# Kernel tuning notes

Hardware: AMD Instinct MI355X
Metric: run time of the kernel (lower is better)

## Reference

```python
import jax, jax.numpy as jnp
import numpy as np

L, H, N, F, E, FF, OUT, B = 4, 8, 1024, 128, 128, 512, 64, 32


def setup_inputs() -> dict:
    key = jax.random.key(0)
    ks = jax.random.split(key, 16)
    s = 0.02
    return {
        "x": jax.random.normal(ks[0], (B, N, F), jnp.float32),
        "adj": jax.random.randint(ks[1], (N, N), 0, 2, jnp.int32),
        "Ws": jax.random.normal(ks[2], (L, H, E, F), jnp.float32) * s,
        "bs": jnp.zeros((L, H, E), jnp.float32),
        "As": jax.random.normal(ks[3], (L, H, 2 * E, N), jnp.float32) * s,
        "W1": jax.random.normal(ks[4], (L, FF, F), jnp.float32) * s,
        "b1": jnp.zeros((L, FF), jnp.float32),
        "W2": jax.random.normal(ks[5], (L, F, FF), jnp.float32) * s,
        "b2": jnp.zeros((L, F), jnp.float32),
        "g1": jnp.ones((L, F), jnp.float32),
        "be1": jnp.zeros((L, F), jnp.float32),
        "g2": jnp.ones((L, F), jnp.float32),
        "be2": jnp.zeros((L, F), jnp.float32),
        "Wo": jax.random.normal(ks[6], (OUT, N * F), jnp.float32) * s,
        "bo": jnp.zeros((OUT,), jnp.float32),
    }


def _ln(x, g, b, eps=1e-5):
    m = jnp.mean(x, axis=-1, keepdims=True)
    v = jnp.mean((x - m) ** 2, axis=-1, keepdims=True)
    return (x - m) / jnp.sqrt(v + eps) * g + b


def reference(x, adj, Ws, bs, As, W1, b1, W2, b2, g1, be1, g2, be2, Wo, bo):
    # mask[j, i] = 1 if j is a neighbor of i (adj_matrix[:, i] > 0 in torch source)
    mask = (adj > 0).astype(x.dtype)
    E_ = Ws.shape[2]
    for l in range(Ws.shape[0]):
        # per-head projection: h [B, H, N, E]
        h = jnp.einsum('bnf,hef->bhne', x, Ws[l]) + bs[l][None, :, None, :]
        # score[b,h,i] = h_i . a[:E, i] + (sum_{j in N(i)} h_j) . a[E:, i]
        s1 = jnp.einsum('bhne,hen->bhn', h, As[l][:, :E_, :])
        hn = jnp.einsum('jn,bhje->bhne', mask, h)  # neighbor sums
        s2 = jnp.einsum('bhne,hen->bhn', hn, As[l][:, E_:, :])
        score = s1 + s2  # [B, H, N]
        # attention row i is the constant score[b,h,i] broadcast over columns,
        # so attention @ h == score[...,None] * h.sum(over nodes)
        hsum = h.sum(axis=2)  # [B, H, E]
        hp = score[..., None] * hsum[:, :, None, :]  # [B, H, N, E]
        att = jax.nn.leaky_relu(hp, 0.01).sum(axis=1)  # sum over heads -> [B, N, F]
        x = _ln(x + att, g1[l], be1[l])
        ff = jax.nn.relu(x @ W1[l].T + b1[l]) @ W2[l].T + b2[l]
        x = _ln(x + ff, g2[l], be2[l])
    flat = x.reshape(x.shape[0], -1)  # [B, N*F]
    return jax.nn.relu(flat) @ Wo.T + bo
```

## Files before the change

### kernel.cpp

```cpp
#include <hip/hip_runtime.h>

#define L_ 4
#define H_ 8
#define Nn 1024
#define F_ 128
#define E_ 128
#define FF_ 512
#define OUT_ 64
#define B_ 32
#define KTOT (Nn * F_)

typedef unsigned short u16;
typedef __bf16 bf16_t;
typedef __attribute__((ext_vector_type(8))) __bf16 bf16x8;
typedef __attribute__((ext_vector_type(4))) float f32x4;

__device__ __forceinline__ u16 f2b(float v) {
    bf16_t h = (bf16_t)v;
    return __builtin_bit_cast(u16, h);
}

typedef const __attribute__((address_space(1))) void* gvp;
typedef __attribute__((address_space(3))) void* lvp;
__device__ __forceinline__ void gll16(const void* g, void* l) {
    __builtin_amdgcn_global_load_lds((gvp)g, (lvp)l, 16, 0, 0);
}

template <int R>
__device__ __forceinline__ void stage(const u16* __restrict__ g, int ldg,
                                      u16* lds, int w, int l) {
    const int r8 = l >> 3, jq = l & 7;
#pragma unroll
    for (int i = 0; i < R / 32; ++i) {
        const int row0 = w * (R / 4) + i * 8;
        const int row = row0 + r8;
        gll16(g + (long)row * ldg + ((jq ^ (row & 7)) << 3), lds + row0 * 64);
    }
}

template <int BM, int BN, bool DUAL, int EPI, int BSH, bool GSWAP, bool DBUF>
__global__ __launch_bounds__(256) void k_mfma(
    const u16* __restrict__ A, int lda, long sAz,
    const u16* __restrict__ Bhp, const u16* __restrict__ Blp, int ldb, long sBz,
    const float* __restrict__ bias,
    float* __restrict__ Cf, u16* __restrict__ Cb, int ldc, long sCz, int K)
{
    constexpr int WN = (BN == 64) ? 1 : ((BM == 64) ? 4 : 2);
    constexpr int WM = 4 / WN;
    constexpr int SM = BM / WM, SN = BN / WN;
    constexpr int MF = SM / 16, NF = SN / 16;
    constexpr int BUFE = BM * 64 + (DUAL ? 2 : 1) * BN * 64;
    __shared__ __align__(16) u16 lds[BUFE * (DBUF ? 2 : 1)];
    const int t = threadIdx.x;
    const int w = t >> 6, l = t & 63, lr = l & 15, lg = l >> 4;
    const int wm0 = (w / WN) * SM, wn0 = (w % WN) * SN;
    const int bidm = GSWAP ? blockIdx.z : blockIdx.x;
    const int bidz = GSWAP ? blockIdx.x : blockIdx.z;
    const int m0 = bidm * BM, n0 = blockIdx.y * BN;
    A += BSH ? ((long)(bidz >> 1) * sAz + (long)(bidz & 1) * 128)
             : (long)bidz * sAz;
    Bhp += (long)(bidz >> BSH) * sBz;
    if (DUAL) Blp += (long)bidz * sBz;

    f32x4 acc[MF][NF] = {};

    auto stageAll = [&](u16* base, int k0) {
        stage<BM>(A + (long)m0 * lda + k0, lda, base, w, l);
        stage<BN>(Bhp + (long)n0 * ldb + k0, ldb, base + BM * 64, w, l);
        if (DUAL) stage<BN>(Blp + (long)n0 * ldb + k0, ldb, base + BM * 64 + BN * 64, w, l);
    };
    auto compute = [&](const u16* base) {
        const u16* Al = base;
        const u16* Bh = base + BM * 64;
        const u16* Bl = Bh + BN * 64;
#pragma unroll
        for (int ks = 0; ks < 2; ++ks) {
            bf16x8 af[MF], bh[NF], bl[NF];
            const int kq = ks * 4 + lg;
#pragma unroll
            for (int mf = 0; mf < MF; ++mf) {
                int row = wm0 + mf * 16 + lr;
                af[mf] = *reinterpret_cast<const bf16x8*>(&Al[row * 64 + ((kq ^ (row & 7)) << 3)]);
            }
#pragma unroll
            for (int nf = 0; nf < NF; ++nf) {
                int row = wn0 + nf * 16 + lr;
                int off = row * 64 + ((kq ^ (row & 7)) << 3);
                bh[nf] = *reinterpret_cast<const bf16x8*>(&Bh[off]);
                if (DUAL) bl[nf] = *reinterpret_cast<const bf16x8*>(&Bl[off]);
            }
#pragma unroll
            for (int mf = 0; mf < MF; ++mf)
#pragma unroll
                for (int nf = 0; nf < NF; ++nf) {
                    acc[mf][nf] = __builtin_amdgcn_mfma_f32_16x16x32_bf16(af[mf], bh[nf], acc[mf][nf], 0, 0, 0);
                    if (DUAL)
                        acc[mf][nf] = __builtin_amdgcn_mfma_f32_16x16x32_bf16(af[mf], bl[nf], acc[mf][nf], 0, 0, 0);
                }
        }
    };

    if (DBUF) {
        stageAll(lds, 0);
        __syncthreads();
        int cur = 0;
        for (int k0 = 0; k0 < K; k0 += 64) {
            if (k0 + 64 < K) stageAll(lds + (cur ^ 1) * BUFE, k0 + 64);
            compute(lds + cur * BUFE);
            __syncthreads();
            cur ^= 1;
        }
    } else {
        for (int k0 = 0; k0 < K; k0 += 64) {
            __syncthreads();
            stageAll(lds, k0);
            __syncthreads();
            compute(lds);
        }
    }

    float bv[NF];
    if (EPI) {
#pragma unroll
        for (int nf = 0; nf < NF; ++nf) bv[nf] = bias[n0 + wn0 + nf * 16 + lr];
    }
    if (EPI == 1) Cb += (long)bidz * sCz;
    else          Cf += (long)bidz * sCz;
#pragma unroll
    for (int mf = 0; mf < MF; ++mf)
#pragma unroll
        for (int nf = 0; nf < NF; ++nf)
#pragma unroll
            for (int r = 0; r < 4; ++r) {
                long row = m0 + wm0 + mf * 16 + lg * 4 + r;
                int col = n0 + wn0 + nf * 16 + lr;
                float v = acc[mf][nf][r];
                if (EPI) v += bv[nf];
                if (EPI == 1) Cb[row * ldc + col] = f2b(fmaxf(v, 0.f));
                else          Cf[row * ldc + col] = v;
            }
}

template <bool LAST>
__global__ __launch_bounds__(256) void k_ff_ln2(
    const u16* __restrict__ xb,
    const u16* __restrict__ W1b,
    const float* __restrict__ b1,
    const u16* __restrict__ W2b,
    const float* __restrict__ b2,
    float* __restrict__ xc,
    const float* __restrict__ g, const float* __restrict__ be,
    u16* __restrict__ xh, u16* __restrict__ xl,
    float* __restrict__ xsp,
    u16* __restrict__ xrb)
{
    __shared__ __align__(16) u16 lds[32768];
    const int t = threadIdx.x;
    const int w = t >> 6, l = t & 63, lr = l & 15, lg = l >> 4;
    const int wn0 = w * 32;
    const int m0 = blockIdx.x * 64;
    u16* A0 = lds;
    u16* P0 = lds + 8192;
    u16* W0 = lds + 16384;

    stage<64>(xb + (long)m0 * F_,      F_, A0, w, l);
    stage<64>(xb + (long)m0 * F_ + 64, F_, A0 + 4096, w, l);

    f32x4 acc2[4][2] = {};
    for (int c = 0; c < 4; ++c) {
        __syncthreads();
        stage<128>(W1b + (long)(c * 128) * F_,      F_, W0, w, l);
        stage<128>(W1b + (long)(c * 128) * F_ + 64, F_, W0 + 8192, w, l);
        __syncthreads();
        f32x4 acc1[4][2] = {};
#pragma unroll
        for (int kh = 0; kh < 2; ++kh) {
            const u16* Ah = A0 + kh * 4096;
            const u16* Wh = W0 + kh * 8192;
#pragma unroll
            for (int ks = 0; ks < 2; ++ks) {
                const int kq = ks * 4 + lg;
                bf16x8 af[4], bfr[2];
#pragma unroll
                for (int mf = 0; mf < 4; ++mf) {
                    int row = mf * 16 + lr;
                    af[mf] = *reinterpret_cast<const bf16x8*>(&Ah[row * 64 + ((kq ^ (row & 7)) << 3)]);
                }
#pragma unroll
                for (int nf = 0; nf < 2; ++nf) {
                    int row = wn0 + nf * 16 + lr;
                    bfr[nf] = *reinterpret_cast<const bf16x8*>(&Wh[row * 64 + ((kq ^ (row & 7)) << 3)]);
                }
#pragma unroll
                for (int mf = 0; mf < 4; ++mf)
#pragma unroll
                    for (int nf = 0; nf < 2; ++nf)
                        acc1[mf][nf] = __builtin_amdgcn_mfma_f32_16x16x32_bf16(af[mf], bfr[nf], acc1[mf][nf], 0, 0, 0);
            }
        }
        float b1v[2] = { b1[c * 128 + wn0 + lr], b1[c * 128 + wn0 + 16 + lr] };
#pragma unroll
        for (int mf = 0; mf < 4; ++mf)
#pragma unroll
            for (int nf = 0; nf < 2; ++nf)
#pragma unroll
                for (int r = 0; r < 4; ++r) {
                    int row = mf * 16 + lg * 4 + r;
                    int cc = wn0 + nf * 16 + lr;
                    int c6 = cc & 63;
                    float v = fmaxf(acc1[mf][nf][r] + b1v[nf], 0.f);
                    P0[(cc >> 6) * 4096 + row * 64 + ((((c6 >> 3) ^ (row & 7))) << 3) + (c6 & 7)] = f2b(v);
                }
        __syncthreads();
        stage<128>(W2b + c * 128,      FF_, W0, w, l);
        stage<128>(W2b + c * 128 + 64, FF_, W0 + 8192, w, l);
        __syncthreads();
#pragma unroll
        for (int kh = 0; kh < 2; ++kh) {
            const u16* Ph = P0 + kh * 4096;
            const u16* Wh = W0 + kh * 8192;
#pragma unroll
            for (int ks = 0; ks < 2; ++ks) {
                const int kq = ks * 4 + lg;
                bf16x8 af[4], bfr[2];
#pragma unroll
                for (int mf = 0; mf < 4; ++mf) {
                    int row = mf * 16 + lr;
                    af[mf] = *reinterpret_cast<const bf16x8*>(&Ph[row * 64 + ((kq ^ (row & 7)) << 3)]);
                }
#pragma unroll
                for (int nf = 0; nf < 2; ++nf) {
                    int row = wn0 + nf * 16 + lr;
                    bfr[nf] = *reinterpret_cast<const bf16x8*>(&Wh[row * 64 + ((kq ^ (row & 7)) << 3)]);
                }
#pragma unroll
                for (int mf = 0; mf < 4; ++mf)
#pragma unroll
                    for (int nf = 0; nf < 2; ++nf)
                        acc2[mf][nf] = __builtin_amdgcn_mfma_f32_16x16x32_bf16(af[mf], bfr[nf], acc2[mf][nf], 0, 0, 0);
            }
        }
    }
    __syncthreads();
    float (*buf)[132] = (float(*)[132])lds;
    float (*ps)[128]  = (float(*)[128])((char*)lds + 34816);
    float bv[2] = { b2[wn0 + lr], b2[wn0 + 16 + lr] };
#pragma unroll
    for (int mf = 0; mf < 4; ++mf)
#pragma unroll
        for (int nf = 0; nf < 2; ++nf)
#pragma unroll
            for (int r = 0; r < 4; ++r)
                buf[mf * 16 + lg * 4 + r][wn0 + nf * 16 + lr] = acc2[mf][nf][r] + bv[nf];
    __syncthreads();
    const float gl0 = g[l], gl1 = g[l + 64], bl0 = be[l], bl1 = be[l + 64];
    float s0 = 0.f, s1 = 0.f;
#pragma unroll
    for (int rr = 0; rr < 16; ++rr) {
        const int row = w * 16 + rr;
        const long xb_ = (long)(m0 + row) * F_;
        float v0 = buf[row][l] + xc[xb_ + l];
        float v1 = buf[row][l + 64] + xc[xb_ + l + 64];
        float sum = v0 + v1;
#pragma unroll
        for (int o = 32; o; o >>= 1) sum += __shfl_xor(sum, o);
        const float mean = sum * (1.f / 128.f);
        const float d0 = v0 - mean, d1 = v1 - mean;
        float vs = d0 * d0 + d1 * d1;
#pragma unroll
        for (int o = 32; o; o >>= 1) vs += __shfl_xor(vs, o);
        const float rstd = rsqrtf(vs * (1.f / 128.f) + 1e-5f);
        float o0 = d0 * rstd * gl0 + bl0;
        float o1 = d1 * rstd * gl1 + bl1;
        if (LAST) {
            xrb[xb_ + l] = f2b(fmaxf(o0, 0.f));
            xrb[xb_ + l + 64] = f2b(fmaxf(o1, 0.f));
        } else {
            xc[xb_ + l] = o0;       xc[xb_ + l + 64] = o1;
            buf[row][l] = o0;       buf[row][l + 64] = o1;
            s0 += o0;               s1 += o1;
        }
    }
    if (!LAST) {
        ps[w][l] = s0; ps[w][l + 64] = s1;
        __syncthreads();
        const int b = m0 >> 10, nb0 = m0 & 1023, seg = (m0 >> 6) & 15;
        const int n8 = (t & 7) * 8, fb = t >> 3;
#pragma unroll
        for (int i = 0; i < 4; ++i) {
            const int f = fb + 32 * i;
            union { u16 u[8]; float4 v; } Hv, Lv;
#pragma unroll
            for (int j = 0; j < 8; ++j) {
                float v = buf[n8 + j][f];
                bf16_t h = (bf16_t)v;
                Hv.u[j] = __builtin_bit_cast(u16, h);
                Lv.u[j] = f2b(v - (float)h);
            }
            const long ob = ((long)b * F_ + f) * Nn + nb0 + n8;
            *reinterpret_cast<float4*>(&xh[ob]) = Hv.v;
            *reinterpret_cast<float4*>(&xl[ob]) = Lv.v;
        }
        if (t < 128)
            xsp[((long)b * 16 + seg) * 128 + t] =
                ps[0][t] + ps[1][t] + ps[2][t] + ps[3][t];
    }
}

__global__ __launch_bounds__(256) void k_final_mfma(
    const u16* __restrict__ xrb, const u16* __restrict__ Wob,
    float* __restrict__ part)
{
    __shared__ __align__(16) u16 Al[32 * 512];
    const int c = blockIdx.x;
    const long k0 = (long)c * 512;
    const int t = threadIdx.x, w = t >> 6, l = t & 63, lr = l & 15, lg = l >> 4;
#pragma unroll
    for (int i = 0; i < 8; ++i) {
        int ch = i * 256 + t, row = ch >> 6, jq = ch & 63;
        *reinterpret_cast<float4*>(&Al[row * 512 + ((jq ^ (row & 7)) << 3)]) =
            *reinterpret_cast<const float4*>(&xrb[(long)row * KTOT + k0 + (jq << 3)]);
    }
    __syncthreads();
    f32x4 acc[2] = {};
    const u16* Bp = Wob + (long)(w * 16 + lr) * KTOT + k0 + lg * 8;
#pragma unroll
    for (int ks = 0; ks < 16; ++ks) {
        bf16x8 bfr = *reinterpret_cast<const bf16x8*>(Bp + ks * 32);
        const int j8 = ks * 4 + lg;
#pragma unroll
        for (int mf = 0; mf < 2; ++mf) {
            int row = mf * 16 + lr;
            bf16x8 af = *reinterpret_cast<const bf16x8*>(&Al[row * 512 + ((j8 ^ (row & 7)) << 3)]);
            acc[mf] = __builtin_amdgcn_mfma_f32_16x16x32_bf16(af, bfr, acc[mf], 0, 0, 0);
        }
    }
#pragma unroll
    for (int mf = 0; mf < 2; ++mf)
#pragma unroll
        for (int r = 0; r < 4; ++r) {
            int b = mf * 16 + lg * 4 + r, o = w * 16 + lr;
            part[((long)c * B_ + b) * OUT_ + o] = acc[mf][r];
        }
}

__global__ void k_final_reduce(const float* __restrict__ part,
                               const float* __restrict__ bo, float* __restrict__ out)
{
    int i = blockIdx.x * 256 + threadIdx.x;
    int o = i & 63;
    float s = bo[o];
    for (int c = 0; c < 256; ++c) s += part[(long)c * (B_ * OUT_) + i];
    out[i] = s;
}

__global__ __launch_bounds__(256) void k_maskT(const int* __restrict__ adj,
                                               u16* __restrict__ maskTb,
                                               int* __restrict__ degi)
{
    __shared__ u16 tl[64][65];
    const int j0 = blockIdx.x * 64, n0 = blockIdx.y * 64, t = threadIdx.x;
#pragma unroll
    for (int i = 0; i < 16; ++i) {
        int s = i * 256 + t, jl = s >> 6, nl = s & 63;
        tl[jl][nl] = (adj[(long)(j0 + jl) * Nn + n0 + nl] > 0) ? 0x3F80 : 0;
    }
    __syncthreads();
    if (t < 64) {
        int c = 0;
#pragma unroll
        for (int jl = 0; jl < 64; ++jl) c += (tl[jl][t] != 0);
        atomicAdd(&degi[n0 + t], c);
    }
#pragma unroll
    for (int i = 0; i < 16; ++i) {
        int s = i * 256 + t, nl = s >> 6, jl = s & 63;
        maskTb[(long)(n0 + nl) * Nn + j0 + jl] = tl[jl][nl];
    }
}

__global__ __launch_bounds__(256) void k_tpb(const float* __restrict__ in,
                                             u16* __restrict__ out, int R, int C)
{
    __shared__ float tl[64][65];
    const int c0 = blockIdx.x * 64, r0 = blockIdx.y * 64, t = threadIdx.x;
    in  += (long)blockIdx.z * R * C;
    out += (long)blockIdx.z * R * C;
#pragma unroll
    for (int i = 0; i < 16; ++i) {
        int s = i * 256 + t, rl = s >> 6, cl = s & 63;
        tl[rl][cl] = in[(long)(r0 + rl) * C + c0 + cl];
    }
    __syncthreads();
#pragma unroll
    for (int i = 0; i < 16; ++i) {
        int s = i * 256 + t, cl = s >> 6, rl = s & 63;
        out[(long)(c0 + cl) * R + r0 + rl] = f2b(tl[rl][cl]);
    }
}

__global__ void k_cvtW(const float* __restrict__ W1, const float* __restrict__ W2,
                       u16* __restrict__ W1b, u16* __restrict__ W2b)
{
    int i = blockIdx.x * 256 + threadIdx.x;
    W1b[i] = f2b(W1[i]);
    W2b[i] = f2b(W2[i]);
}

__global__ void k_cvtWo(const float* __restrict__ Wo, u16* __restrict__ Wob)
{
    long i = ((long)blockIdx.x * 256 + threadIdx.x) * 8;
    float4 a = *reinterpret_cast<const float4*>(&Wo[i]);
    float4 b = *reinterpret_cast<const float4*>(&Wo[i + 4]);
    union { u16 u[8]; float4 v; } r;
    r.u[0] = f2b(a.x); r.u[1] = f2b(a.y); r.u[2] = f2b(a.z); r.u[3] = f2b(a.w);
    r.u[4] = f2b(b.x); r.u[5] = f2b(b.y); r.u[6] = f2b(b.z); r.u[7] = f2b(b.w);
    *reinterpret_cast<float4*>(&Wob[i]) = r.v;
}

__global__ __launch_bounds__(256) void k_xpose(const float* __restrict__ x,
                                               u16* __restrict__ xh, u16* __restrict__ xl)
{
    __shared__ float tile[64][132];
    const int b = blockIdx.y, n0 = blockIdx.x * 64, t = threadIdx.x;
#pragma unroll
    for (int i = 0; i < 8; ++i) {
        int s = i * 256 + t, nl = s >> 5, f4 = (s & 31) << 2;
        float4 v = *reinterpret_cast<const float4*>(&x[((long)b * Nn + n0 + nl) * F_ + f4]);
        tile[nl][f4] = v.x; tile[nl][f4 + 1] = v.y;
        tile[nl][f4 + 2] = v.z; tile[nl][f4 + 3] = v.w;
    }
    __syncthreads();
    const int f = t >> 1, nb = (t & 1) << 5;
    const long ob = ((long)b * F_ + f) * Nn + n0 + nb;
    union { u16 u[8]; float4 v; } Hv, Lv;
#pragma unroll
    for (int i = 0; i < 32; i += 8) {
#pragma unroll
        for (int j = 0; j < 8; ++j) {
            float v = tile[nb + i + j][f];
            bf16_t h = (bf16_t)v;
            Hv.u[j] = __builtin_bit_cast(u16, h);
            Lv.u[j] = f2b(v - (float)h);
        }
        *reinterpret_cast<float4*>(&xh[ob + i]) = Hv.v;
        *reinterpret_cast<float4*>(&xl[ob + i]) = Lv.v;
    }
}

__global__ __launch_bounds__(256) void k_xs2(const float* __restrict__ x, float* __restrict__ xsp)
{
    __shared__ float sh[2][128];
    const int seg = blockIdx.x, b = blockIdx.y, t = threadIdx.x;
    const int f = t & 127, h2 = t >> 7;
    const float* p = x + ((long)b * Nn + seg * 64 + h2 * 32) * F_ + f;
    float s = 0.f;
    for (int i = 0; i < 32; ++i) s += p[(long)i * F_];
    sh[h2][f] = s;
    __syncthreads();
    if (t < 128) xsp[((long)b * 16 + seg) * 128 + t] = sh[0][t] + sh[1][t];
}

__global__ void k_hsum(const float* __restrict__ xsp, const float* __restrict__ Wl,
                       const float* __restrict__ bsl, float* __restrict__ hsum)
{
    __shared__ float xs[128];
    const int i = blockIdx.x * 256 + threadIdx.x;
    const int b = i >> 10;
    if (threadIdx.x < 128) {
        const float* xp = xsp + (long)b * 16 * 128 + threadIdx.x;
        float v = 0.f;
#pragma unroll
        for (int sg = 0; sg < 16; ++sg) v += xp[sg * 128];
        xs[threadIdx.x] = v;
    }
    __syncthreads();
    const int e = i & 127, h = (i >> 7) & 7;
    const float* w = Wl + ((long)h * E_ + e) * F_;
    float s = 0.f;
    for (int f = 0; f < F_; ++f) s += xs[f] * w[f];
    hsum[i] = s + (float)Nn * bsl[h * E_ + e];
}

__global__ void k_d12(const float* __restrict__ As, const float* __restrict__ bs,
                      float* __restrict__ d12all)
{
    const int lyr = blockIdx.y;
    const float* Asl = As + (long)lyr * H_ * 2 * E_ * Nn;
    const float* bsl = bs + (long)lyr * H_ * E_;
    int i = blockIdx.x * 256 + threadIdx.x;
    int n = i & 1023, h = (i >> 10) & 7, w = i >> 13;
    const float* a = Asl + ((long)h * 2 * E_ + (long)w * E_) * Nn + n;
    const float* bb = bsl + h * E_;
    float s = 0.f;
    for (int e = 0; e < E_; ++e) s += bb[e] * a[(long)e * Nn];
    d12all[(long)lyr * 2 * H_ * Nn + ((long)w * H_ + h) * Nn + n] = s;
}

__global__ __launch_bounds__(256) void k_score_ln1(
    float* __restrict__ x, const float* __restrict__ y,
    const float* __restrict__ Ct, const float* __restrict__ d12,
    const int* __restrict__ degi, const float* __restrict__ hsum,
    const float* __restrict__ g, const float* __restrict__ be,
    u16* __restrict__ xb)
{
    const int n = blockIdx.x, t = threadIdx.x;
    __shared__ float c1[H_][128], c2[H_][128];
    __shared__ float sbs[H_];
#pragma unroll
    for (int i = 0; i < 4; ++i) {
        int s = i * 256 + t, h = s >> 7, f = s & 127;
        c1[h][f] = Ct[((long)(2 * h) * Nn + n) * F_ + f];
        c2[h][f] = Ct[((long)(2 * h + 1) * Nn + n) * F_ + f];
    }
    if (t < H_) sbs[t] = d12[(long)t * Nn + n] + (float)degi[n] * d12[(long)(H_ + t) * Nn + n];
    __syncthreads();
    const int w = t >> 6, l = t & 63;
    const float gl0 = g[l], gl1 = g[l + 64], bl0 = be[l], bl1 = be[l + 64];
    for (int bi = 0; bi < 8; ++bi) {
        const int b = w * 8 + bi;
        const long base = ((long)b * Nn + n) * F_;
        float x0 = x[base + l], x1 = x[base + l + 64];
        float y0 = y[base + l], y1 = y[base + l + 64];
        float a0 = 0.f, a1 = 0.f;
#pragma unroll
        for (int h = 0; h < H_; ++h) {
            float p = x0 * c1[h][l] + x1 * c1[h][l + 64]
                    + y0 * c2[h][l] + y1 * c2[h][l + 64];
#pragma unroll
            for (int o = 32; o; o >>= 1) p += __shfl_xor(p, o);
            float s = p + sbs[h];
            float h0 = hsum[((long)b * H_ + h) * E_ + l];
            float h1 = hsum[((long)b * H_ + h) * E_ + l + 64];
            float p0 = s * h0, p1 = s * h1;
            a0 += (p0 > 0.f ? p0 : 0.01f * p0);
            a1 += (p1 > 0.f ? p1 : 0.01f * p1);
        }
        float v0 = x0 + a0, v1 = x1 + a1;
        float sum = v0 + v1;
#pragma unroll
        for (int o = 32; o; o >>= 1) sum += __shfl_xor(sum, o);
        const float mean = sum * (1.f / 128.f);
        const float d0 = v0 - mean, d1 = v1 - mean;
        float vs = d0 * d0 + d1 * d1;
#pragma unroll
        for (int o = 32; o; o >>= 1) vs += __shfl_xor(vs, o);
        const float rstd = rsqrtf(vs * (1.f / 128.f) + 1e-5f);
        float o0 = d0 * rstd * gl0 + bl0;
        float o1 = d1 * rstd * gl1 + bl1;
        x[base + l] = o0;        x[base + l + 64] = o1;
        xb[base + l] = f2b(o0);  xb[base + l + 64] = f2b(o1);
    }
}

extern "C" void kernel_launch(void* const* d_in, const int* in_sizes, int n_in,
                              void* d_out, int out_size, void* d_ws, size_t ws_size,
                              hipStream_t stream)
{
    const float* x_in = (const float*)d_in[0];
    const int*   adj  = (const int*)d_in[1];
    const float* Ws   = (const float*)d_in[2];
    const float* bs   = (const float*)d_in[3];
    const float* As   = (const float*)d_in[4];
    const float* W1   = (const float*)d_in[5];
    const float* b1   = (const float*)d_in[6];
    const float* W2   = (const float*)d_in[7];
    const float* b2   = (const float*)d_in[8];
    const float* g1   = (const float*)d_in[9];
    const float* be1  = (const float*)d_in[10];
    const float* g2   = (const float*)d_in[11];
    const float* be2  = (const float*)d_in[12];
    const float* Wo   = (const float*)d_in[13];
    const float* bo   = (const float*)d_in[14];
    float* out = (float*)d_out;

    char* wsb = (char*)d_ws;
    u16*   maskTb = (u16*)wsb;
    float* xc     = (float*)(wsb + (2L << 20));
    float* y      = (float*)(wsb + (18L << 20));
    float* CtAll  = (float*)(wsb + (66L << 20));
    u16*   xb     = (u16*)(wsb + (98L << 20));
    u16*   xrb    = (u16*)(wsb + (106L << 20));
    u16*   Wob    = (u16*)(wsb + (114L << 20));
    float* part   = (float*)(wsb + (130L << 20));
    u16*   xTh    = (u16*)(wsb + (132L << 20));
    u16*   xTl    = (u16*)(wsb + (140L << 20));
    u16*   AsTb   = (u16*)(wsb + (148L << 20));
    u16*   WsTb   = (u16*)(wsb + (164L << 20));
    char*  S      = wsb + (166L << 20);
    int*   degi   = (int*)S;
    float* xsp    = (float*)(S + (4L << 10));
    float* hsum   = (float*)(S + (260L << 10));
    float* d12all = (float*)(S + (388L << 10));
    u16*   W1b    = (u16*)(S + (644L << 10));
    u16*   W2b    = (u16*)(S + (1156L << 10));

    hipMemsetAsync(degi, 0, Nn * sizeof(int), stream);
    hipMemcpyAsync(xc, x_in, sizeof(float) * (long)B_ * Nn * F_,
                   hipMemcpyDeviceToDevice, stream);
    k_maskT<<<dim3(16, 16), 256, 0, stream>>>(adj, maskTb, degi);
    k_cvtW<<<(L_ * FF_ * F_) / 256, 256, 0, stream>>>(W1, W2, W1b, W2b);
    k_cvtWo<<<(OUT_ * KTOT) / (256 * 8), 256, 0, stream>>>(Wo, Wob);
    k_tpb<<<dim3(16, 4, L_ * H_), 256, 0, stream>>>(As, AsTb, 2 * E_, Nn);
    k_tpb<<<dim3(2, 2, L_ * H_), 256, 0, stream>>>(Ws, WsTb, E_, F_);
    k_xpose<<<dim3(16, B_), 256, 0, stream>>>(x_in, xTh, xTl);
    k_xs2<<<dim3(16, B_), 256, 0, stream>>>(x_in, xsp);
    k_d12<<<dim3((2 * H_ * Nn) / 256, L_), 256, 0, stream>>>(As, bs, d12all);
    k_mfma<64, 128, false, 0, 1, false, false><<<dim3(16, 1, 64), 256, 0, stream>>>(
        AsTb, 2 * E_, (long)Nn * 2 * E_, WsTb, nullptr, E_, (long)F_ * E_,
        nullptr, CtAll, nullptr, F_, (long)Nn * F_, E_);

    for (int l = 0; l < L_; ++l) {
        const float* Wl  = Ws + (long)l * H_ * E_ * F_;
        const float* bsl = bs + (long)l * H_ * E_;

        k_mfma<128, 64, true, 0, 0, true, true><<<dim3(32, 2, 8), 256, 0, stream>>>(
            maskTb, Nn, 0L, xTh, xTl, Nn, (long)F_ * Nn,
            nullptr, y, nullptr, F_, (long)Nn * F_, Nn);

        k_hsum<<<(B_ * H_ * E_) / 256, 256, 0, stream>>>(xsp, Wl, bsl, hsum);
        k_score_ln1<<<Nn, 256, 0, stream>>>(
            xc, y, CtAll + (long)l * 16 * Nn * F_, d12all + (long)l * 2 * H_ * Nn,
            degi, hsum, g1 + l * F_, be1 + l * F_, xb);
        if (l < L_ - 1)
            k_ff_ln2<false><<<512, 256, 0, stream>>>(
                xb, W1b + (long)l * FF_ * F_, b1 + l * FF_,
                W2b + (long)l * F_ * FF_, b2 + l * F_, xc,
                g2 + l * F_, be2 + l * F_, xTh, xTl, xsp, nullptr);
        else
            k_ff_ln2<true><<<512, 256, 0, stream>>>(
                xb, W1b + (long)l * FF_ * F_, b1 + l * FF_,
                W2b + (long)l * F_ * FF_, b2 + l * F_, xc,
                g2 + l * F_, be2 + l * F_, nullptr, nullptr, nullptr, xrb);
    }

    k_final_mfma<<<256, 256, 0, stream>>>(xrb, Wob, part);
    k_final_reduce<<<(B_ * OUT_) / 256, 256, 0, stream>>>(part, bo, out);
}
```

Measured before the change: 394.2 us.

## Prefetch FFN weight tiles into registers to overlap with MFMA compute

Replaces the synchronous LDS staging of W1/W2 tiles in the fused FFN kernel with a register prefetch. The next weight tile is loaded from global memory into registers while the current GEMM runs, then written to LDS after a barrier, so global load latency hides behind the matrix-multiply work. It also changes the XOR swizzle on the P buffer to mix in row>>3, which should reduce LDS bank conflicts. The cost is higher register pressure from 8 float4 prefetch registers, which may lower occupancy, plus some reordering of barriers.

```diff
diff --git a/kernel.cpp b/kernel.cpp
--- a/kernel.cpp
+++ b/kernel.cpp
@@ -162,16 +162,39 @@
     u16* A0 = lds;
     u16* P0 = lds + 8192;
     u16* W0 = lds + 16384;
+    const int r8 = l >> 3, jq = l & 7;
+
+    float4 wreg[8];
+    auto loadW = [&](const u16* Wsrc, int ld) {
+#pragma unroll
+        for (int h = 0; h < 2; ++h)
+#pragma unroll
+            for (int i = 0; i < 4; ++i) {
+                int row = w * 32 + i * 8 + r8;
+                wreg[h * 4 + i] = *reinterpret_cast<const float4*>(
+                    &Wsrc[(long)row * ld + h * 64 + ((jq ^ (row & 7)) << 3)]);
+            }
+    };
+    auto writeW = [&]() {
+#pragma unroll
+        for (int h = 0; h < 2; ++h)
+#pragma unroll
+            for (int i = 0; i < 4; ++i) {
+                int row0 = w * 32 + i * 8;
+                *reinterpret_cast<float4*>(&W0[h * 8192 + row0 * 64 + l * 8]) = wreg[h * 4 + i];
+            }
+    };
 
     stage<64>(xb + (long)m0 * F_,      F_, A0, w, l);
     stage<64>(xb + (long)m0 * F_ + 64, F_, A0 + 4096, w, l);
+    loadW(W1b, F_);
+    __syncthreads();
+    writeW();
 
     f32x4 acc2[4][2] = {};
     for (int c = 0; c < 4; ++c) {
         __syncthreads();
-        stage<128>(W1b + (long)(c * 128) * F_,      F_, W0, w, l);
-        stage<128>(W1b + (long)(c * 128) * F_ + 64, F_, W0 + 8192, w, l);
-        __syncthreads();
+        loadW(W2b + c * 128, FF_);
         f32x4 acc1[4][2] = {};
 #pragma unroll
         for (int kh = 0; kh < 2; ++kh) {
@@ -198,6 +221,8 @@
                         acc1[mf][nf] = __builtin_amdgcn_mfma_f32_16x16x32_bf16(af[mf], bfr[nf], acc1[mf][nf], 0, 0, 0);
             }
         }
+        __syncthreads();
+        writeW();
         float b1v[2] = { b1[c * 128 + wn0 + lr], b1[c * 128 + wn0 + 16 + lr] };
 #pragma unroll
         for (int mf = 0; mf < 4; ++mf)
@@ -206,14 +231,13 @@
 #pragma unroll
                 for (int r = 0; r < 4; ++r) {
                     int row = mf * 16 + lg * 4 + r;
+                    int sp = (row ^ (row >> 3)) & 7;
                     int cc = wn0 + nf * 16 + lr;
                     int c6 = cc & 63;
                     float v = fmaxf(acc1[mf][nf][r] + b1v[nf], 0.f);
-                    P0[(cc >> 6) * 4096 + row * 64 + ((((c6 >> 3) ^ (row & 7))) << 3) + (c6 & 7)] = f2b(v);
+                    P0[(cc >> 6) * 4096 + row * 64 + (((c6 >> 3) ^ sp) << 3) + (c6 & 7)] = f2b(v);
                 }
-        __syncthreads();
-        stage<128>(W2b + c * 128,      FF_, W0, w, l);
-        stage<128>(W2b + c * 128 + 64, FF_, W0 + 8192, w, l);
+        if (c < 3) loadW(W1b + (long)(c + 1) * 128 * F_, F_);
         __syncthreads();
 #pragma unroll
         for (int kh = 0; kh < 2; ++kh) {
@@ -226,7 +250,8 @@
 #pragma unroll
                 for (int mf = 0; mf < 4; ++mf) {
                     int row = mf * 16 + lr;
-                    af[mf] = *reinterpret_cast<const bf16x8*>(&Ph[row * 64 + ((kq ^ (row & 7)) << 3)]);
+                    int sp = (row ^ (row >> 3)) & 7;
+                    af[mf] = *reinterpret_cast<const bf16x8*>(&Ph[row * 64 + ((kq ^ sp) << 3)]);
                 }
 #pragma unroll
                 for (int nf = 0; nf < 2; ++nf) {
@@ -240,8 +265,9 @@
                         acc2[mf][nf] = __builtin_amdgcn_mfma_f32_16x16x32_bf16(af[mf], bfr[nf], acc2[mf][nf], 0, 0, 0);
             }
         }
-    }
-    __syncthreads();
+        __syncthreads();
+        if (c < 3) writeW();
+    }
     float (*buf)[132] = (float(*)[132])lds;
     float (*ps)[128]  = (float(*)[128])((char*)lds + 34816);
     float bv[2] = { b2[wn0 + lr], b2[wn0 + 16 + lr] };
```

Result: slower. 497.7 us (+26.3%).

## Drop split-bf16 low part for neighbor-sum GEMM and store its output in bf16

Applied to the files above, without the earlier changes.

The mask-times-x neighbor-sum GEMM previously used a hi/lo bf16 split of x, doubling the MFMA work and the transposed-x traffic. It now uses only the bf16 high part, drops the xTl buffer from the transpose and LN2 kernels, and writes the result y as bf16 instead of fp32, which halves its store and load traffic. The LDS swizzle for the P tile in the FF kernel is also changed to reduce bank conflicts. The cost is lower accuracy in the neighbor sums, which may push the output closer to the tolerance limit.

```diff
diff --git a/kernel.cpp b/kernel.cpp
--- a/kernel.cpp
+++ b/kernel.cpp
@@ -18,6 +18,10 @@
 __device__ __forceinline__ u16 f2b(float v) {
     bf16_t h = (bf16_t)v;
     return __builtin_bit_cast(u16, h);
+}
+__device__ __forceinline__ float b2f(u16 u) {
+    unsigned v = (unsigned)u << 16;
+    return __builtin_bit_cast(float, v);
 }
 
 typedef const __attribute__((address_space(1))) void* gvp;
@@ -120,12 +124,12 @@
     }
 
     float bv[NF];
-    if (EPI) {
+    if (EPI == 1) {
 #pragma unroll
         for (int nf = 0; nf < NF; ++nf) bv[nf] = bias[n0 + wn0 + nf * 16 + lr];
     }
-    if (EPI == 1) Cb += (long)bidz * sCz;
-    else          Cf += (long)bidz * sCz;
+    if (EPI == 1 || EPI == 3) Cb += (long)bidz * sCz;
+    else                      Cf += (long)bidz * sCz;
 #pragma unroll
     for (int mf = 0; mf < MF; ++mf)
 #pragma unroll
@@ -135,9 +139,9 @@
                 long row = m0 + wm0 + mf * 16 + lg * 4 + r;
                 int col = n0 + wn0 + nf * 16 + lr;
                 float v = acc[mf][nf][r];
-                if (EPI) v += bv[nf];
-                if (EPI == 1) Cb[row * ldc + col] = f2b(fmaxf(v, 0.f));
-                else          Cf[row * ldc + col] = v;
+                if (EPI == 1) Cb[row * ldc + col] = f2b(fmaxf(v + bv[nf], 0.f));
+                else if (EPI == 3) Cb[row * ldc + col] = f2b(v);
+                else Cf[row * ldc + col] = v;
             }
 }
 
@@ -150,7 +154,7 @@
     const float* __restrict__ b2,
     float* __restrict__ xc,
     const float* __restrict__ g, const float* __restrict__ be,
-    u16* __restrict__ xh, u16* __restrict__ xl,
+    u16* __restrict__ xh,
     float* __restrict__ xsp,
     u16* __restrict__ xrb)
 {
@@ -206,10 +210,11 @@
 #pragma unroll
                 for (int r = 0; r < 4; ++r) {
                     int row = mf * 16 + lg * 4 + r;
+                    int sp = (row ^ (row >> 3)) & 7;
                     int cc = wn0 + nf * 16 + lr;
                     int c6 = cc & 63;
                     float v = fmaxf(acc1[mf][nf][r] + b1v[nf], 0.f);
-                    P0[(cc >> 6) * 4096 + row * 64 + ((((c6 >> 3) ^ (row & 7))) << 3) + (c6 & 7)] = f2b(v);
+                    P0[(cc >> 6) * 4096 + row * 64 + (((c6 >> 3) ^ sp) << 3) + (c6 & 7)] = f2b(v);
                 }
         __syncthreads();
         stage<128>(W2b + c * 128,      FF_, W0, w, l);
@@ -226,7 +231,8 @@
 #pragma unroll
                 for (int mf = 0; mf < 4; ++mf) {
                     int row = mf * 16 + lr;
-                    af[mf] = *reinterpret_cast<const bf16x8*>(&Ph[row * 64 + ((kq ^ (row & 7)) << 3)]);
+                    int sp = (row ^ (row >> 3)) & 7;
+                    af[mf] = *reinterpret_cast<const bf16x8*>(&Ph[row * 64 + ((kq ^ sp) << 3)]);
                 }
 #pragma unroll
                 for (int nf = 0; nf < 2; ++nf) {
@@ -289,17 +295,10 @@
 #pragma unroll
         for (int i = 0; i < 4; ++i) {
             const int f = fb + 32 * i;
-            union { u16 u[8]; float4 v; } Hv, Lv;
-#pragma unroll
-            for (int j = 0; j < 8; ++j) {
-                float v = buf[n8 + j][f];
-                bf16_t h = (bf16_t)v;
-                Hv.u[j] = __builtin_bit_cast(u16, h);
-                Lv.u[j] = f2b(v - (float)h);
-            }
-            const long ob = ((long)b * F_ + f) * Nn + nb0 + n8;
-            *reinterpret_cast<float4*>(&xh[ob]) = Hv.v;
-            *reinterpret_cast<float4*>(&xl[ob]) = Lv.v;
+            union { u16 u[8]; float4 v; } Hv;
+#pragma unroll
+            for (int j = 0; j < 8; ++j) Hv.u[j] = f2b(buf[n8 + j][f]);
+            *reinterpret_cast<float4*>(&xh[((long)b * F_ + f) * Nn + nb0 + n8]) = Hv.v;
         }
         if (t < 128)
             xsp[((long)b * 16 + seg) * 128 + t] =
@@ -419,7 +418,7 @@
 }
 
 __global__ __launch_bounds__(256) void k_xpose(const float* __restrict__ x,
-                                               u16* __restrict__ xh, u16* __restrict__ xl)
+                                               u16* __restrict__ xh)
 {
     __shared__ float tile[64][132];
     const int b = blockIdx.y, n0 = blockIdx.x * 64, t = threadIdx.x;
@@ -433,18 +432,12 @@
     __syncthreads();
     const int f = t >> 1, nb = (t & 1) << 5;
     const long ob = ((long)b * F_ + f) * Nn + n0 + nb;
-    union { u16 u[8]; float4 v; } Hv, Lv;
+    union { u16 u[8]; float4 v; } Hv;
 #pragma unroll
     for (int i = 0; i < 32; i += 8) {
 #pragma unroll
-        for (int j = 0; j < 8; ++j) {
-            float v = tile[nb + i + j][f];
-            bf16_t h = (bf16_t)v;
-            Hv.u[j] = __builtin_bit_cast(u16, h);
-            Lv.u[j] = f2b(v - (float)h);
-        }
+        for (int j = 0; j < 8; ++j) Hv.u[j] = f2b(tile[nb + i + j][f]);
         *reinterpret_cast<float4*>(&xh[ob + i]) = Hv.v;
-        *reinterpret_cast<float4*>(&xl[ob + i]) = Lv.v;
     }
 }
 
@@ -498,7 +491,7 @@
 }
 
 __global__ __launch_bounds__(256) void k_score_ln1(
-    float* __restrict__ x, const float* __restrict__ y,
+    float* __restrict__ x, const u16* __restrict__ y,
     const float* __restrict__ Ct, const float* __restrict__ d12,
     const int* __restrict__ degi, const float* __restrict__ hsum,
     const float* __restrict__ g, const float* __restrict__ be,
@@ -521,7 +514,7 @@
         const int b = w * 8 + bi;
         const long base = ((long)b * Nn + n) * F_;
         float x0 = x[base + l], x1 = x[base + l + 64];
-        float y0 = y[base + l], y1 = y[base + l + 64];
+        float y0 = b2f(y[base + l]), y1 = b2f(y[base + l + 64]);
         float a0 = 0.f, a1 = 0.f;
 #pragma unroll
         for (int h = 0; h < H_; ++h) {
@@ -577,14 +570,13 @@
     char* wsb = (char*)d_ws;
     u16*   maskTb = (u16*)wsb;
     float* xc     = (float*)(wsb + (2L << 20));
-    float* y      = (float*)(wsb + (18L << 20));
+    u16*   yb     = (u16*)(wsb + (18L << 20));
     float* CtAll  = (float*)(wsb + (66L << 20));
     u16*   xb     = (u16*)(wsb + (98L << 20));
     u16*   xrb    = (u16*)(wsb + (106L << 20));
     u16*   Wob    = (u16*)(wsb + (114L << 20));
     float* part   = (float*)(wsb + (130L << 20));
     u16*   xTh    = (u16*)(wsb + (132L << 20));
-    u16*   xTl    = (u16*)(wsb + (140L << 20));
     u16*   AsTb   = (u16*)(wsb + (148L << 20));
     u16*   WsTb   = (u16*)(wsb + (164L << 20));
     char*  S      = wsb + (166L << 20);
@@ -603,7 +595,7 @@
     k_cvtWo<<<(OUT_ * KTOT) / (256 * 8), 256, 0, stream>>>(Wo, Wob);
     k_tpb<<<dim3(16, 4, L_ * H_), 256, 0, stream>>>(As, AsTb, 2 * E_, Nn);
     k_tpb<<<dim3(2, 2, L_ * H_), 256, 0, stream>>>(Ws, WsTb, E_, F_);
-    k_xpose<<<dim3(16, B_), 256, 0, stream>>>(x_in, xTh, xTl);
+    k_xpose<<<dim3(16, B_), 256, 0, stream>>>(x_in, xTh);
     k_xs2<<<dim3(16, B_), 256, 0, stream>>>(x_in, xsp);
     k_d12<<<dim3((2 * H_ * Nn) / 256, L_), 256, 0, stream>>>(As, bs, d12all);
     k_mfma<64, 128, false, 0, 1, false, false><<<dim3(16, 1, 64), 256, 0, stream>>>(
@@ -614,24 +606,24 @@
         const float* Wl  = Ws + (long)l * H_ * E_ * F_;
         const float* bsl = bs + (long)l * H_ * E_;
 
-        k_mfma<128, 64, true, 0, 0, true, true><<<dim3(32, 2, 8), 256, 0, stream>>>(
-            maskTb, Nn, 0L, xTh, xTl, Nn, (long)F_ * Nn,
-            nullptr, y, nullptr, F_, (long)Nn * F_, Nn);
+        k_mfma<128, 64, false, 3, 0, true, true><<<dim3(32, 2, 8), 256, 0, stream>>>(
+            maskTb, Nn, 0L, xTh, nullptr, Nn, (long)F_ * Nn,
+            nullptr, nullptr, yb, F_, (long)Nn * F_, Nn);
 
         k_hsum<<<(B_ * H_ * E_) / 256, 256, 0, stream>>>(xsp, Wl, bsl, hsum);
         k_score_ln1<<<Nn, 256, 0, stream>>>(
-            xc, y, CtAll + (long)l * 16 * Nn * F_, d12all + (long)l * 2 * H_ * Nn,
+            xc, yb, CtAll + (long)l * 16 * Nn * F_, d12all + (long)l * 2 * H_ * Nn,
             degi, hsum, g1 + l * F_, be1 + l * F_, xb);
         if (l < L_ - 1)
             k_ff_ln2<false><<<512, 256, 0, stream>>>(
                 xb, W1b + (long)l * FF_ * F_, b1 + l * FF_,
                 W2b + (long)l * F_ * FF_, b2 + l * F_, xc,
-                g2 + l * F_, be2 + l * F_, xTh, xTl, xsp, nullptr);
+                g2 + l * F_, be2 + l * F_, xTh, xsp, nullptr);
         else
             k_ff_ln2<true><<<512, 256, 0, stream>>>(
                 xb, W1b + (long)l * FF_ * F_, b1 + l * FF_,
                 W2b + (long)l * F_ * FF_, b2 + l * F_, xc,
-                g2 + l * F_, be2 + l * F_, nullptr, nullptr, nullptr, xrb);
+                g2 + l * F_, be2 + l * F_, nullptr, nullptr, xrb);
     }
 
     k_final_mfma<<<256, 256, 0, stream>>>(xrb, Wob, part);
```

Measured after the change: 368.5 us. 1.07x faster.
